# Kernel optimization log

Measured on AMD Instinct MI355X. Metric: run time of the kernel, lower is better.

## Reference

```python
import jax, jax.numpy as jnp
import numpy as np

N_NODES = 50000
N_EDGES = 800000
D_FEAT = 64      # num_src_feats == num_dst_feats
D_EDGE = 16      # num_edge_feats
D_HID = 16       # hidden width of both tiny MLPs
D_MSG = 64       # msg_size
D_OUT = 64       # num_out_feats


def setup_inputs() -> dict:
    key = jax.random.key(0)
    ks = jax.random.split(key, 12)
    x = jax.random.normal(ks[0], (N_NODES, D_FEAT), dtype=jnp.float32)
    edge_feats = jax.random.normal(ks[1], (N_EDGES, D_EDGE), dtype=jnp.float32)
    src = jax.random.randint(ks[2], (N_EDGES,), 0, N_NODES, dtype=jnp.int32)
    dst = jax.random.randint(ks[3], (N_EDGES,), 0, N_NODES, dtype=jnp.int32)

    def linear_params(k, fan_in, fan_out):
        kw, kb = jax.random.split(k)
        bound = 1.0 / np.sqrt(fan_in)
        W = jax.random.uniform(kw, (fan_in, fan_out), jnp.float32, -bound, bound)
        b = jax.random.uniform(kb, (fan_out,), jnp.float32, -bound, bound)
        return W, b

    # fc_msg: [D_EDGE + D_FEAT, 16, D_MSG]
    msg_W1, msg_b1 = linear_params(ks[4], D_EDGE + D_FEAT, D_HID)
    msg_W2, msg_b2 = linear_params(ks[5], D_HID, D_MSG)
    # fc_udt: [D_FEAT + D_MSG, 16, D_OUT]
    udt_W1, udt_b1 = linear_params(ks[6], D_FEAT + D_MSG, D_HID)
    udt_W2, udt_b2 = linear_params(ks[7], D_HID, D_OUT)

    return {
        "x": x, "edge_feats": edge_feats, "src": src, "dst": dst,
        "msg_W1": msg_W1, "msg_b1": msg_b1, "msg_W2": msg_W2, "msg_b2": msg_b2,
        "udt_W1": udt_W1, "udt_b1": udt_b1, "udt_W2": udt_W2, "udt_b2": udt_b2,
    }


def reference(x, edge_feats, src, dst,
              msg_W1, msg_b1, msg_W2, msg_b2,
              udt_W1, udt_b1, udt_W2, udt_b2):
    # message: m_e = MLP([edge_feats_e, x[src_e]])   (cat order: edge first)
    edge_in = jnp.concatenate([edge_feats, x[src]], axis=1)  # [E, D_EDGE+D_FEAT]
    h = jax.nn.relu(edge_in @ msg_W1 + msg_b1)
    m = h @ msg_W2 + msg_b2  # [E, D_MSG]

    # reduce: r_v = max over incoming edges (DGL fills 0 for nodes w/o in-edges)
    r = jax.ops.segment_max(m, dst, num_segments=N_NODES)  # [N, D_MSG]
    r = jnp.where(jnp.isfinite(r), r, 0.0)

    # update: out_v = MLP([x_v, r_v])
    upd_in = jnp.concatenate([x, r], axis=1)  # [N, D_FEAT+D_MSG]
    h2 = jax.nn.relu(upd_in @ udt_W1 + udt_b1)
    return h2 @ udt_W2 + udt_b2  # [N, D_OUT]
```

## Files before the change

### kernel.cpp

```cpp
#include <hip/hip_runtime.h>
#include <hip/hip_fp16.h>

#define N_NODES 50000
#define N_EDGES 800000

#define NBu 1568
#define BSH 5
#define PB  512
#define EPB 1563
#define PIT 7
#define NCH 7

__device__ __forceinline__ unsigned fkey(float f) {
    unsigned u = __float_as_uint(f);
    return (u & 0x80000000u) ? ~u : (u | 0x80000000u);
}
#define KEY_NEG_INF 0x007FFFFFu

__device__ __forceinline__ unsigned block_exscan256(unsigned v, unsigned* wsum,
                                                    unsigned* chunkTot) {
    const int t = threadIdx.x, lane = t & 63, w = t >> 6;
    unsigned inc = v;
#pragma unroll
    for (int d = 1; d < 64; d <<= 1) {
        unsigned n = __shfl_up(inc, d, 64);
        if (lane >= d) inc += n;
    }
    if (lane == 63) wsum[w] = inc;
    __syncthreads();
    unsigned woff = 0;
#pragma unroll
    for (int i = 0; i < 3; ++i) if (i < w) woff += wsum[i];
    if (chunkTot && t == 255) *chunkTot = woff + inc;
    __syncthreads();
    return woff + inc - v;
}

__global__ __launch_bounds__(256) void chist_xw_kernel(
    const int* __restrict__ dst, unsigned* __restrict__ bcnt,
    const float* __restrict__ x, const float* __restrict__ W1,
    const float* __restrict__ b1, float* __restrict__ xw)
{
    __shared__ unsigned lh[NBu];
    const int t = threadIdx.x, b = blockIdx.x;
    for (int i = t; i < NBu; i += 256) lh[i] = 0u;
    __syncthreads();
    const int e0 = b * EPB;
#pragma unroll
    for (int it = 0; it < PIT; ++it) {
        const int i = it * 256 + t;
        const int e = e0 + i;
        if (i < EPB && e < N_EDGES) atomicAdd(&lh[(unsigned)dst[e] >> BSH], 1u);
    }
    __syncthreads();
    for (int i = t; i < NBu; i += 256) bcnt[(size_t)b * NBu + i] = lh[i];

    if (b < 196) {
        const int v = b * 256 + t;
        if (v < N_NODES) {
            float acc[16];
#pragma unroll
            for (int k = 0; k < 16; ++k) acc[k] = b1[k];
            const float4* xp = reinterpret_cast<const float4*>(x) + (size_t)v * 16;
#pragma unroll
            for (int c = 0; c < 16; ++c) {
                float4 tv = xp[c];
                const float xv[4] = {tv.x, tv.y, tv.z, tv.w};
#pragma unroll
                for (int q = 0; q < 4; ++q) {
                    const int row = 16 + 4 * c + q;
#pragma unroll
                    for (int k = 0; k < 16; ++k)
                        acc[k] = fmaf(xv[q], W1[row * 16 + k], acc[k]);
                }
            }
            float4* op = reinterpret_cast<float4*>(xw) + (size_t)v * 4;
#pragma unroll
            for (int c = 0; c < 4; ++c) {
                float4 o; o.x = acc[4*c]; o.y = acc[4*c+1]; o.z = acc[4*c+2]; o.w = acc[4*c+3];
                op[c] = o;
            }
        }
    }
}

__global__ __launch_bounds__(256) void cscanA_kernel(const unsigned* __restrict__ bcnt,
                                                     unsigned* __restrict__ gstart,
                                                     unsigned* __restrict__ tot) {
    __shared__ unsigned wsum[4];
    __shared__ unsigned carrySh, chunkTot;
    const int t = threadIdx.x, bu = blockIdx.x;
    if (t == 0) carrySh = 0u;
    __syncthreads();
#pragma unroll
    for (int c = 0; c < PB / 256; ++c) {
        const int k = c * 256 + t;
        const unsigned v = bcnt[(size_t)k * NBu + bu];
        const unsigned excl = block_exscan256(v, wsum, &chunkTot);
        gstart[(size_t)k * NBu + bu] = carrySh + excl;
        __syncthreads();
        if (t == 0) carrySh += chunkTot;
        __syncthreads();
    }
    if (t == 0) tot[bu] = carrySh;
}

__global__ __launch_bounds__(256) void cscanB_kernel(const unsigned* __restrict__ tot,
                                                     unsigned* __restrict__ boffG) {
    __shared__ unsigned wsum[4];
    __shared__ unsigned carrySh, chunkTot;
    const int t = threadIdx.x;
    if (t == 0) carrySh = 0u;
    __syncthreads();
    for (int c = 0; c < NCH; ++c) {
        const int idx = c * 256 + t;
        const unsigned v = (idx < NBu) ? tot[idx] : 0u;
        const unsigned excl = block_exscan256(v, wsum, &chunkTot);
        if (idx < NBu) boffG[idx] = carrySh + excl;
        __syncthreads();
        if (t == 0) carrySh += chunkTot;
        __syncthreads();
    }
}

__global__ __launch_bounds__(256) void partition_kernel(
    const int* __restrict__ dst, const unsigned* __restrict__ gstart,
    const unsigned* __restrict__ boffG, unsigned* __restrict__ part)
{
    __shared__ unsigned stV[EPB];
    __shared__ unsigned short stB[EPB];
    __shared__ unsigned lh[NBu], lstart[NBu], lc[NBu], gs[NBu];
    __shared__ unsigned wsum[4], carrySh, chunkTot;
    const int t = threadIdx.x, b = blockIdx.x;
    for (int i = t; i < NBu; i += 256) lh[i] = 0u;
    __syncthreads();
    const int e0 = b * EPB;
#pragma unroll
    for (int it = 0; it < PIT; ++it) {
        const int i = it * 256 + t;
        const int e = e0 + i;
        if (i < EPB && e < N_EDGES) atomicAdd(&lh[(unsigned)dst[e] >> BSH], 1u);
    }
    if (t == 0) carrySh = 0u;
    __syncthreads();
    for (int c = 0; c < NCH; ++c) {
        const int idx = c * 256 + t;
        const unsigned v = (idx < NBu) ? lh[idx] : 0u;
        const unsigned excl = block_exscan256(v, wsum, &chunkTot);
        if (idx < NBu) {
            const unsigned s0 = carrySh + excl;
            lstart[idx] = s0;
            lc[idx]     = s0;
            gs[idx]     = gstart[(size_t)b * NBu + idx] + boffG[idx];
        }
        __syncthreads();
        if (t == 0) carrySh += chunkTot;
        __syncthreads();
    }
#pragma unroll
    for (int it = 0; it < PIT; ++it) {
        const int i = it * 256 + t;
        const int e = e0 + i;
        if (i < EPB && e < N_EDGES) {
            const unsigned d = (unsigned)dst[e];
            const unsigned bkt = d >> BSH;
            const unsigned p = atomicAdd(&lc[bkt], 1u);
            stV[p] = ((d & 31u) << 20) | (unsigned)e;
            stB[p] = (unsigned short)bkt;
        }
    }
    __syncthreads();
    const int lim = min(EPB, N_EDGES - e0);
#pragma unroll
    for (int it = 0; it < PIT; ++it) {
        const int i = it * 256 + t;
        if (i < lim) {
            const unsigned bkt = stB[i];
            part[gs[bkt] + ((unsigned)i - lstart[bkt])] = stV[i];
        }
    }
}

__global__ __launch_bounds__(256) void hcomp_kernel(
    const float* __restrict__ ef, const int* __restrict__ src,
    const float* __restrict__ xw, const float* __restrict__ W1,
    unsigned* __restrict__ h16)
{
    const int e = blockIdx.x * 256 + threadIdx.x;
    float in[16];
    const float4* efp = reinterpret_cast<const float4*>(ef) + (size_t)e * 4;
#pragma unroll
    for (int c = 0; c < 4; ++c) {
        float4 tv = efp[c];
        in[4*c+0]=tv.x; in[4*c+1]=tv.y; in[4*c+2]=tv.z; in[4*c+3]=tv.w;
    }
    const int s = src[e];
    float h[16];
    const float4* xp = reinterpret_cast<const float4*>(xw) + (size_t)s * 4;
#pragma unroll
    for (int c = 0; c < 4; ++c) {
        float4 tv = xp[c];
        h[4*c+0]=tv.x; h[4*c+1]=tv.y; h[4*c+2]=tv.z; h[4*c+3]=tv.w;
    }
#pragma unroll
    for (int i = 0; i < 16; ++i)
#pragma unroll
        for (int k = 0; k < 16; ++k)
            h[k] = fmaf(in[i], W1[i*16 + k], h[k]);
    unsigned wds[8];
#pragma unroll
    for (int k = 0; k < 8; ++k) {
        __half2 t2 = __floats2half2_rn(fmaxf(h[2*k], 0.0f), fmaxf(h[2*k+1], 0.0f));
        wds[k] = *reinterpret_cast<unsigned*>(&t2);
    }
    uint4* hp = reinterpret_cast<uint4*>(h16) + (size_t)e * 2;
    hp[0] = make_uint4(wds[0], wds[1], wds[2], wds[3]);
    hp[1] = make_uint4(wds[4], wds[5], wds[6], wds[7]);
}

__global__ __launch_bounds__(256) void reduce_fused_kernel(
    const unsigned* __restrict__ part,
    const unsigned* __restrict__ boffG, const unsigned* __restrict__ tot,
    const unsigned* __restrict__ h16,
    const float* __restrict__ W2, const float* __restrict__ b2,
    const float* __restrict__ x,
    const float* __restrict__ uW1, const float* __restrict__ ub1,
    const float* __restrict__ uW2, const float* __restrict__ ub2,
    float* __restrict__ out)
{
    __shared__ unsigned rmax[32][65];
    __shared__ float    xsh[32][65];
    const int tid = threadIdx.x, b = blockIdx.x;
    const unsigned base = boffG[b], cnt = tot[b];
    const int v0 = b * 32;

    for (int i = tid; i < 32 * 65; i += 256) (&rmax[0][0])[i] = KEY_NEG_INF;
    for (int i = tid; i < 512; i += 256) {
        const int row = i >> 4, c = i & 15;
        float4 tv = (v0 + row < N_NODES)
            ? reinterpret_cast<const float4*>(x)[(size_t)(v0 + row) * 16 + c]
            : make_float4(0.f, 0.f, 0.f, 0.f);
        xsh[row][c*4+0] = tv.x; xsh[row][c*4+1] = tv.y;
        xsh[row][c*4+2] = tv.z; xsh[row][c*4+3] = tv.w;
    }
    __syncthreads();

    const int nIter = (int)((cnt + 255u) >> 8);
    for (int it = 0; it < nIter; ++it) {
        const unsigned slot = (unsigned)it * 256u + (unsigned)tid;
        if (slot < cnt) {
            const unsigned pv = part[base + slot];
            const int e    = (int)(pv & 0xFFFFFu);
            const int nloc = (int)(pv >> 20);
            float h[16];
            {
                const uint4* hp = reinterpret_cast<const uint4*>(h16) + (size_t)e * 2;
                uint4 A = hp[0], B = hp[1];
                unsigned wd[8] = {A.x, A.y, A.z, A.w, B.x, B.y, B.z, B.w};
#pragma unroll
                for (int k = 0; k < 8; ++k) {
                    __half2 t2 = *reinterpret_cast<const __half2*>(&wd[k]);
                    float2 f = __half22float2(t2);
                    h[2*k] = f.x; h[2*k+1] = f.y;
                }
            }
#pragma unroll
            for (int j0 = 0; j0 < 64; j0 += 16) {
                float m[16];
#pragma unroll
                for (int t16 = 0; t16 < 16; ++t16) m[t16] = b2[j0 + t16];
#pragma unroll
                for (int k = 0; k < 16; ++k)
#pragma unroll
                    for (int t16 = 0; t16 < 16; ++t16)
                        m[t16] = fmaf(h[k], W2[k*64 + j0 + t16], m[t16]);
#pragma unroll
                for (int t16 = 0; t16 < 16; ++t16)
                    atomicMax(&rmax[nloc][j0 + t16], fkey(m[t16]));
            }
        }
    }
    __syncthreads();

    if (tid < 128) {
        const int nl = tid >> 2;
        const int qq = tid & 3;
        const int v  = v0 + nl;
        if (v < N_NODES) {
            float h2[16];
#pragma unroll
            for (int k = 0; k < 16; ++k) h2[k] = ub1[k];
            for (int row = 0; row < 64; ++row) {
                const float xv = xsh[nl][row];
#pragma unroll
                for (int k = 0; k < 16; ++k)
                    h2[k] = fmaf(xv, uW1[row*16 + k], h2[k]);
            }
            for (int j = 0; j < 64; ++j) {
                const unsigned kk = rmax[nl][j];
                unsigned u = (kk & 0x80000000u) ? (kk ^ 0x80000000u) : ~kk;
                float f = __uint_as_float(u);
                if (!(f >= -3.402823466e38f && f <= 3.402823466e38f)) f = 0.0f;
#pragma unroll
                for (int k = 0; k < 16; ++k)
                    h2[k] = fmaf(f, uW1[(64 + j)*16 + k], h2[k]);
            }
#pragma unroll
            for (int k = 0; k < 16; ++k) h2[k] = fmaxf(h2[k], 0.0f);
            float* op = out + (size_t)v * 64 + qq * 16;
#pragma unroll
            for (int c = 0; c < 4; ++c) {
                float oo[4];
#pragma unroll
                for (int u4 = 0; u4 < 4; ++u4) {
                    const int col = qq*16 + 4*c + u4;
                    float a = ub2[col];
#pragma unroll
                    for (int k = 0; k < 16; ++k)
                        a = fmaf(h2[k], uW2[k*64 + col], a);
                    oo[u4] = a;
                }
                float4 o; o.x=oo[0]; o.y=oo[1]; o.z=oo[2]; o.w=oo[3];
                reinterpret_cast<float4*>(op)[c] = o;
            }
        }
    }
}

__device__ __forceinline__ void wave_lds_fence() {
    asm volatile("s_waitcnt lgkmcnt(0)" ::: "memory");
    __builtin_amdgcn_sched_barrier(0);
}

__global__ __launch_bounds__(256) void init0_kernel(unsigned* __restrict__ rkey) {
    const int i = blockIdx.x * 256 + threadIdx.x;
    reinterpret_cast<uint4*>(rkey)[i] =
        make_uint4(KEY_NEG_INF, KEY_NEG_INF, KEY_NEG_INF, KEY_NEG_INF);
}

__global__ __launch_bounds__(64) void edge_kernel(
    const float* __restrict__ x, const float* __restrict__ ef,
    const int* __restrict__ src, const int* __restrict__ dst,
    const float* __restrict__ W1, const float* __restrict__ b1,
    const float* __restrict__ W2, const float* __restrict__ b2,
    unsigned* __restrict__ rkey)
{
    const int lane = threadIdx.x;
    const int e    = blockIdx.x * 64 + lane;
    __shared__ unsigned mld[64][17];
    __shared__ int      dld[64];
    float in[80];
    const float4* efp = reinterpret_cast<const float4*>(ef) + (size_t)e * 4;
#pragma unroll
    for (int c = 0; c < 4; ++c) {
        float4 tv = efp[c];
        in[4*c+0]=tv.x; in[4*c+1]=tv.y; in[4*c+2]=tv.z; in[4*c+3]=tv.w;
    }
    const int s = src[e];
    dld[lane] = dst[e];
    const float4* xp = reinterpret_cast<const float4*>(x) + (size_t)s * 16;
#pragma unroll
    for (int c = 0; c < 16; ++c) {
        float4 tv = xp[c];
        in[16+4*c+0]=tv.x; in[16+4*c+1]=tv.y; in[16+4*c+2]=tv.z; in[16+4*c+3]=tv.w;
    }
    float h[16];
#pragma unroll
    for (int k = 0; k < 16; ++k) h[k] = b1[k];
#pragma unroll
    for (int i = 0; i < 80; ++i)
#pragma unroll
        for (int k = 0; k < 16; ++k)
            h[k] = fmaf(in[i], W1[i*16 + k], h[k]);
#pragma unroll
    for (int k = 0; k < 16; ++k) h[k] = fmaxf(h[k], 0.0f);
    const int er = lane >> 4, jj = lane & 15;
#pragma unroll
    for (int j0 = 0; j0 < 64; j0 += 16) {
        float m[16];
#pragma unroll
        for (int t = 0; t < 16; ++t) m[t] = b2[j0 + t];
#pragma unroll
        for (int k = 0; k < 16; ++k)
#pragma unroll
            for (int t = 0; t < 16; ++t)
                m[t] = fmaf(h[k], W2[k*64 + j0 + t], m[t]);
        wave_lds_fence();
#pragma unroll
        for (int t = 0; t < 16; ++t) mld[lane][t] = fkey(m[t]);
        wave_lds_fence();
#pragma unroll
        for (int eg = 0; eg < 16; ++eg) {
            const int ee = (eg << 2) | er;
            atomicMax(&rkey[((size_t)dld[ee] << 6) + (unsigned)(j0 + jj)],
                      mld[ee][jj]);
        }
    }
}

__global__ __launch_bounds__(256) void node_kernel(
    const float* __restrict__ x, const unsigned* rkey,
    const float* __restrict__ W1, const float* __restrict__ b1,
    const float* __restrict__ W2, const float* __restrict__ b2,
    float* out)
{
    const int v = blockIdx.x * 256 + threadIdx.x;
    if (v >= N_NODES) return;
    float in[128];
    const float4* xp = reinterpret_cast<const float4*>(x) + (size_t)v * 16;
#pragma unroll
    for (int c = 0; c < 16; ++c) {
        float4 tv = xp[c];
        in[4*c+0]=tv.x; in[4*c+1]=tv.y; in[4*c+2]=tv.z; in[4*c+3]=tv.w;
    }
    const uint4* rp = reinterpret_cast<const uint4*>(rkey) + (size_t)v * 16;
#pragma unroll
    for (int c = 0; c < 16; ++c) {
        uint4 tv = rp[c];
        unsigned ks[4] = {tv.x, tv.y, tv.z, tv.w};
#pragma unroll
        for (int qq = 0; qq < 4; ++qq) {
            unsigned k = ks[qq];
            unsigned u = (k & 0x80000000u) ? (k ^ 0x80000000u) : ~k;
            float f = __uint_as_float(u);
            if (!(f >= -3.402823466e38f && f <= 3.402823466e38f)) f = 0.0f;
            in[64 + 4*c + qq] = f;
        }
    }
    float h[16];
#pragma unroll
    for (int k = 0; k < 16; ++k) h[k] = b1[k];
#pragma unroll
    for (int i = 0; i < 128; ++i)
#pragma unroll
        for (int k = 0; k < 16; ++k)
            h[k] = fmaf(in[i], W1[i*16 + k], h[k]);
#pragma unroll
    for (int k = 0; k < 16; ++k) h[k] = fmaxf(h[k], 0.0f);
    float* op = out + (size_t)v * 64;
#pragma unroll
    for (int c = 0; c < 16; ++c) {
        float oo[4];
#pragma unroll
        for (int qq = 0; qq < 4; ++qq) {
            float a = b2[4*c + qq];
#pragma unroll
            for (int k = 0; k < 16; ++k)
                a = fmaf(h[k], W2[k*64 + 4*c + qq], a);
            oo[qq] = a;
        }
        float4 o; o.x=oo[0]; o.y=oo[1]; o.z=oo[2]; o.w=oo[3];
        reinterpret_cast<float4*>(op)[c] = o;
    }
}

extern "C" void kernel_launch(void* const* d_in, const int* in_sizes, int n_in,
                              void* d_out, int out_size, void* d_ws, size_t ws_size,
                              hipStream_t stream) {
    const float* x   = (const float*)d_in[0];
    const float* ef  = (const float*)d_in[1];
    const int*   src = (const int*)d_in[2];
    const int*   dst = (const int*)d_in[3];
    const float* mW1 = (const float*)d_in[4];
    const float* mb1 = (const float*)d_in[5];
    const float* mW2 = (const float*)d_in[6];
    const float* mb2 = (const float*)d_in[7];
    const float* uW1 = (const float*)d_in[8];
    const float* ub1 = (const float*)d_in[9];
    const float* uW2 = (const float*)d_in[10];
    const float* ub2 = (const float*)d_in[11];

    float* out = (float*)d_out;

    unsigned* part   = (unsigned*)d_ws;
    unsigned* bcnt   = part + N_EDGES;
    unsigned* gstart = bcnt + (size_t)PB * NBu;
    unsigned* tot    = gstart + (size_t)PB * NBu;
    unsigned* boffG  = tot + NBu;
    float*    xw     = (float*)(boffG + NBu);
    unsigned* h16    = (unsigned*)(xw + (size_t)50176 * 16);
    const size_t T1_NEEDED =
        (size_t)((char*)(h16 + (size_t)N_EDGES * 8) - (char*)d_ws);

    if (ws_size >= T1_NEEDED) {
        hipLaunchKernelGGL(chist_xw_kernel,  dim3(PB),   dim3(256), 0, stream,
                           dst, bcnt, x, mW1, mb1, xw);
        hipLaunchKernelGGL(cscanA_kernel,    dim3(NBu),  dim3(256), 0, stream,
                           bcnt, gstart, tot);
        hipLaunchKernelGGL(cscanB_kernel,    dim3(1),    dim3(256), 0, stream,
                           tot, boffG);
        hipLaunchKernelGGL(partition_kernel, dim3(PB),   dim3(256), 0, stream,
                           dst, gstart, boffG, part);
        hipLaunchKernelGGL(hcomp_kernel,     dim3(3125), dim3(256), 0, stream,
                           ef, src, xw, mW1, h16);
        hipLaunchKernelGGL(reduce_fused_kernel, dim3(NBu), dim3(256), 0, stream,
                           part, boffG, tot, h16, mW2, mb2,
                           x, uW1, ub1, uW2, ub2, out);
    } else {
        unsigned* rkey = (unsigned*)d_out;
        hipLaunchKernelGGL(init0_kernel, dim3(3125), dim3(256), 0, stream, rkey);
        hipLaunchKernelGGL(edge_kernel, dim3(12500), dim3(64), 0, stream,
                           x, ef, src, dst, mW1, mb1, mW2, mb2, rkey);
        hipLaunchKernelGGL(node_kernel, dim3((N_NODES + 255) / 256), dim3(256), 0, stream,
                           x, rkey, uW1, ub1, uW2, ub2, out);
    }
}
```

Before: 124.5 us.

## Build full CSR by destination with two-level partition and per-node register max reduction

Replaces the single-level 32-node bucket partition and LDS atomicMax reduction with a two-pass partition: 256-node coarse buckets, then a per-bucket counting sort by node to build a full CSR (nbase offsets). The reduce kernel now assigns 8 lanes per node, computes messages and keeps the max in registers, combines with shuffles, and fuses the update MLP. This removes LDS atomics and the 2-D scan but adds an extra partition pass, more register pressure (64-float accumulators), and per-node load imbalance.

```diff
diff --git a/kernel.cpp b/kernel.cpp
--- a/kernel.cpp
+++ b/kernel.cpp
@@ -4,18 +4,23 @@
 #define N_NODES 50000
 #define N_EDGES 800000
 
-#define NBu 1568
-#define BSH 5
-#define PB  512
-#define EPB 1563
-#define PIT 7
-#define NCH 7
+#define NB   196
+#define PB   256
+#define EPB  3125
+#define PIT  13
+#define CAP2 4608
+#define NVT  50176
 
 __device__ __forceinline__ unsigned fkey(float f) {
     unsigned u = __float_as_uint(f);
     return (u & 0x80000000u) ? ~u : (u | 0x80000000u);
 }
 #define KEY_NEG_INF 0x007FFFFFu
+
+__device__ __forceinline__ void wave_lds_fence() {
+    asm volatile("s_waitcnt lgkmcnt(0)" ::: "memory");
+    __builtin_amdgcn_sched_barrier(0);
+}
 
 __device__ __forceinline__ unsigned block_exscan256(unsigned v, unsigned* wsum,
                                                     unsigned* chunkTot) {
@@ -41,19 +46,18 @@
     const float* __restrict__ x, const float* __restrict__ W1,
     const float* __restrict__ b1, float* __restrict__ xw)
 {
-    __shared__ unsigned lh[NBu];
+    __shared__ unsigned lh[NB];
     const int t = threadIdx.x, b = blockIdx.x;
-    for (int i = t; i < NBu; i += 256) lh[i] = 0u;
+    if (t < NB) lh[t] = 0u;
     __syncthreads();
     const int e0 = b * EPB;
 #pragma unroll
     for (int it = 0; it < PIT; ++it) {
         const int i = it * 256 + t;
-        const int e = e0 + i;
-        if (i < EPB && e < N_EDGES) atomicAdd(&lh[(unsigned)dst[e] >> BSH], 1u);
-    }
-    __syncthreads();
-    for (int i = t; i < NBu; i += 256) bcnt[(size_t)b * NBu + i] = lh[i];
+        if (i < EPB) atomicAdd(&lh[(unsigned)dst[e0 + i] >> 8], 1u);
+    }
+    __syncthreads();
+    if (t < NB) bcnt[(size_t)b * NB + t] = lh[t];
 
     if (b < 196) {
         const int v = b * 256 + t;
@@ -84,101 +88,23 @@
     }
 }
 
-__global__ __launch_bounds__(256) void cscanA_kernel(const unsigned* __restrict__ bcnt,
-                                                     unsigned* __restrict__ gstart,
+__global__ __launch_bounds__(256) void cscanA_kernel(unsigned* __restrict__ bcnt,
                                                      unsigned* __restrict__ tot) {
     __shared__ unsigned wsum[4];
-    __shared__ unsigned carrySh, chunkTot;
     const int t = threadIdx.x, bu = blockIdx.x;
-    if (t == 0) carrySh = 0u;
-    __syncthreads();
-#pragma unroll
-    for (int c = 0; c < PB / 256; ++c) {
-        const int k = c * 256 + t;
-        const unsigned v = bcnt[(size_t)k * NBu + bu];
-        const unsigned excl = block_exscan256(v, wsum, &chunkTot);
-        gstart[(size_t)k * NBu + bu] = carrySh + excl;
-        __syncthreads();
-        if (t == 0) carrySh += chunkTot;
-        __syncthreads();
-    }
-    if (t == 0) tot[bu] = carrySh;
+    const unsigned v = bcnt[(size_t)t * NB + bu];
+    const unsigned excl = block_exscan256(v, wsum, nullptr);
+    bcnt[(size_t)t * NB + bu] = excl;
+    if (t == 255) tot[bu] = excl + v;
 }
 
 __global__ __launch_bounds__(256) void cscanB_kernel(const unsigned* __restrict__ tot,
                                                      unsigned* __restrict__ boffG) {
     __shared__ unsigned wsum[4];
-    __shared__ unsigned carrySh, chunkTot;
     const int t = threadIdx.x;
-    if (t == 0) carrySh = 0u;
-    __syncthreads();
-    for (int c = 0; c < NCH; ++c) {
-        const int idx = c * 256 + t;
-        const unsigned v = (idx < NBu) ? tot[idx] : 0u;
-        const unsigned excl = block_exscan256(v, wsum, &chunkTot);
-        if (idx < NBu) boffG[idx] = carrySh + excl;
-        __syncthreads();
-        if (t == 0) carrySh += chunkTot;
-        __syncthreads();
-    }
-}
-
-__global__ __launch_bounds__(256) void partition_kernel(
-    const int* __restrict__ dst, const unsigned* __restrict__ gstart,
-    const unsigned* __restrict__ boffG, unsigned* __restrict__ part)
-{
-    __shared__ unsigned stV[EPB];
-    __shared__ unsigned short stB[EPB];
-    __shared__ unsigned lh[NBu], lstart[NBu], lc[NBu], gs[NBu];
-    __shared__ unsigned wsum[4], carrySh, chunkTot;
-    const int t = threadIdx.x, b = blockIdx.x;
-    for (int i = t; i < NBu; i += 256) lh[i] = 0u;
-    __syncthreads();
-    const int e0 = b * EPB;
-#pragma unroll
-    for (int it = 0; it < PIT; ++it) {
-        const int i = it * 256 + t;
-        const int e = e0 + i;
-        if (i < EPB && e < N_EDGES) atomicAdd(&lh[(unsigned)dst[e] >> BSH], 1u);
-    }
-    if (t == 0) carrySh = 0u;
-    __syncthreads();
-    for (int c = 0; c < NCH; ++c) {
-        const int idx = c * 256 + t;
-        const unsigned v = (idx < NBu) ? lh[idx] : 0u;
-        const unsigned excl = block_exscan256(v, wsum, &chunkTot);
-        if (idx < NBu) {
-            const unsigned s0 = carrySh + excl;
-            lstart[idx] = s0;
-            lc[idx]     = s0;
-            gs[idx]     = gstart[(size_t)b * NBu + idx] + boffG[idx];
-        }
-        __syncthreads();
-        if (t == 0) carrySh += chunkTot;
-        __syncthreads();
-    }
-#pragma unroll
-    for (int it = 0; it < PIT; ++it) {
-        const int i = it * 256 + t;
-        const int e = e0 + i;
-        if (i < EPB && e < N_EDGES) {
-            const unsigned d = (unsigned)dst[e];
-            const unsigned bkt = d >> BSH;
-            const unsigned p = atomicAdd(&lc[bkt], 1u);
-            stV[p] = ((d & 31u) << 20) | (unsigned)e;
-            stB[p] = (unsigned short)bkt;
-        }
-    }
-    __syncthreads();
-    const int lim = min(EPB, N_EDGES - e0);
-#pragma unroll
-    for (int it = 0; it < PIT; ++it) {
-        const int i = it * 256 + t;
-        if (i < lim) {
-            const unsigned bkt = stB[i];
-            part[gs[bkt] + ((unsigned)i - lstart[bkt])] = stV[i];
-        }
-    }
+    const unsigned v = (t < NB) ? tot[t] : 0u;
+    const unsigned excl = block_exscan256(v, wsum, nullptr);
+    if (t < NB) boffG[t] = excl;
 }
 
 __global__ __launch_bounds__(256) void hcomp_kernel(
@@ -218,9 +144,103 @@
     hp[1] = make_uint4(wds[4], wds[5], wds[6], wds[7]);
 }
 
-__global__ __launch_bounds__(256) void reduce_fused_kernel(
-    const unsigned* __restrict__ part,
+__global__ __launch_bounds__(256) void part1_kernel(
+    const int* __restrict__ dst, const unsigned* __restrict__ gstart,
+    const unsigned* __restrict__ boffG, unsigned* __restrict__ part1)
+{
+    __shared__ unsigned stV[EPB];
+    __shared__ unsigned char stB[EPB];
+    __shared__ unsigned lh[NB], lstart[NB], lc[NB], gs[NB];
+    __shared__ unsigned wsum[4];
+    const int t = threadIdx.x, b = blockIdx.x;
+    if (t < NB) lh[t] = 0u;
+    __syncthreads();
+    const int e0 = b * EPB;
+#pragma unroll
+    for (int it = 0; it < PIT; ++it) {
+        const int i = it * 256 + t;
+        if (i < EPB) atomicAdd(&lh[(unsigned)dst[e0 + i] >> 8], 1u);
+    }
+    __syncthreads();
+    {
+        const unsigned v = (t < NB) ? lh[t] : 0u;
+        const unsigned excl = block_exscan256(v, wsum, nullptr);
+        if (t < NB) {
+            lstart[t] = excl;
+            lc[t]     = excl;
+            gs[t]     = gstart[(size_t)b * NB + t] + boffG[t];
+        }
+    }
+    __syncthreads();
+#pragma unroll
+    for (int it = 0; it < PIT; ++it) {
+        const int i = it * 256 + t;
+        if (i < EPB) {
+            const int e = e0 + i;
+            const unsigned d = (unsigned)dst[e];
+            const unsigned bkt = d >> 8;
+            const unsigned p = atomicAdd(&lc[bkt], 1u);
+            stV[p] = ((d & 255u) << 20) | (unsigned)e;
+            stB[p] = (unsigned char)bkt;
+        }
+    }
+    __syncthreads();
+#pragma unroll
+    for (int it = 0; it < PIT; ++it) {
+        const int i = it * 256 + t;
+        if (i < EPB) {
+            const unsigned bkt = stB[i];
+            part1[gs[bkt] + ((unsigned)i - lstart[bkt])] = stV[i];
+        }
+    }
+}
+
+__global__ __launch_bounds__(256) void part2_kernel(
+    const unsigned* __restrict__ part1,
     const unsigned* __restrict__ boffG, const unsigned* __restrict__ tot,
+    unsigned* __restrict__ part2, unsigned* __restrict__ nbase)
+{
+    __shared__ unsigned stE[CAP2];
+    __shared__ unsigned fh[256], fstart[256], fcur[256];
+    __shared__ unsigned wsum[4];
+    const int t = threadIdx.x, b = blockIdx.x;
+    const unsigned gb = boffG[b], cnt = tot[b];
+    fh[t] = 0u; fcur[t] = 0u;
+    __syncthreads();
+    const int iters = (int)((cnt + 255u) >> 8);
+    for (int it = 0; it < iters; ++it) {
+        const unsigned i = (unsigned)it * 256u + (unsigned)t;
+        if (i < cnt) atomicAdd(&fh[part1[gb + i] >> 20], 1u);
+    }
+    __syncthreads();
+    {
+        const unsigned v = fh[t];
+        fstart[t] = block_exscan256(v, wsum, nullptr);
+    }
+    __syncthreads();
+    for (int it = 0; it < iters; ++it) {
+        const unsigned i = (unsigned)it * 256u + (unsigned)t;
+        if (i < cnt) {
+            const unsigned pv = part1[gb + i];
+            const unsigned nloc = pv >> 20;
+            const unsigned e = pv & 0xFFFFFu;
+            const unsigned pos = fstart[nloc] + atomicAdd(&fcur[nloc], 1u);
+            if (pos < CAP2) stE[pos] = e;
+            else            part2[gb + pos] = e;
+        }
+    }
+    __syncthreads();
+    const unsigned lim = (cnt < CAP2) ? cnt : CAP2;
+    for (int it = 0; it < iters; ++it) {
+        const unsigned i = (unsigned)it * 256u + (unsigned)t;
+        if (i < lim) part2[gb + i] = stE[i];
+    }
+    nbase[(size_t)b * 256 + t] = gb + fstart[t];
+    if (b == NB - 1 && t == 0) nbase[NVT] = (unsigned)N_EDGES;
+}
+
+__global__ __launch_bounds__(128) void reduce_node_kernel(
+    const unsigned* __restrict__ part2, const unsigned* __restrict__ nbase,
     const unsigned* __restrict__ h16,
     const float* __restrict__ W2, const float* __restrict__ b2,
     const float* __restrict__ x,
@@ -228,108 +248,108 @@
     const float* __restrict__ uW2, const float* __restrict__ ub2,
     float* __restrict__ out)
 {
-    __shared__ unsigned rmax[32][65];
-    __shared__ float    xsh[32][65];
     const int tid = threadIdx.x, b = blockIdx.x;
-    const unsigned base = boffG[b], cnt = tot[b];
-    const int v0 = b * 32;
-
-    for (int i = tid; i < 32 * 65; i += 256) (&rmax[0][0])[i] = KEY_NEG_INF;
-    for (int i = tid; i < 512; i += 256) {
-        const int row = i >> 4, c = i & 15;
-        float4 tv = (v0 + row < N_NODES)
-            ? reinterpret_cast<const float4*>(x)[(size_t)(v0 + row) * 16 + c]
-            : make_float4(0.f, 0.f, 0.f, 0.f);
-        xsh[row][c*4+0] = tv.x; xsh[row][c*4+1] = tv.y;
-        xsh[row][c*4+2] = tv.z; xsh[row][c*4+3] = tv.w;
-    }
-    __syncthreads();
-
-    const int nIter = (int)((cnt + 255u) >> 8);
-    for (int it = 0; it < nIter; ++it) {
-        const unsigned slot = (unsigned)it * 256u + (unsigned)tid;
-        if (slot < cnt) {
-            const unsigned pv = part[base + slot];
-            const int e    = (int)(pv & 0xFFFFFu);
-            const int nloc = (int)(pv >> 20);
+    const int g = tid >> 3, l = tid & 7;
+    const int v = b * 16 + g;
+    if (v >= N_NODES) return;
+
+    const unsigned beg = nbase[v], end = nbase[v + 1];
+    float acc[64];
+#pragma unroll
+    for (int j = 0; j < 64; ++j) acc[j] = -__builtin_inff();
+
+    const unsigned deg = end - beg;
+    const int trips = (int)((deg + 7u) >> 3);
+    for (int tr = 0; tr < trips; ++tr) {
+        const unsigned idx = beg + (unsigned)tr * 8u + (unsigned)l;
+        if (idx < end) {
+            const unsigned e = part2[idx];
+            const uint4* hp = reinterpret_cast<const uint4*>(h16) + (size_t)e * 2;
+            uint4 A = hp[0], B = hp[1];
+            unsigned wd[8] = {A.x, A.y, A.z, A.w, B.x, B.y, B.z, B.w};
             float h[16];
-            {
-                const uint4* hp = reinterpret_cast<const uint4*>(h16) + (size_t)e * 2;
-                uint4 A = hp[0], B = hp[1];
-                unsigned wd[8] = {A.x, A.y, A.z, A.w, B.x, B.y, B.z, B.w};
-#pragma unroll
-                for (int k = 0; k < 8; ++k) {
-                    __half2 t2 = *reinterpret_cast<const __half2*>(&wd[k]);
-                    float2 f = __half22float2(t2);
-                    h[2*k] = f.x; h[2*k+1] = f.y;
-                }
+#pragma unroll
+            for (int k = 0; k < 8; ++k) {
+                __half2 t2 = *reinterpret_cast<const __half2*>(&wd[k]);
+                float2 f = __half22float2(t2);
+                h[2*k] = f.x; h[2*k+1] = f.y;
             }
 #pragma unroll
-            for (int j0 = 0; j0 < 64; j0 += 16) {
-                float m[16];
-#pragma unroll
-                for (int t16 = 0; t16 < 16; ++t16) m[t16] = b2[j0 + t16];
-#pragma unroll
-                for (int k = 0; k < 16; ++k)
-#pragma unroll
-                    for (int t16 = 0; t16 < 16; ++t16)
-                        m[t16] = fmaf(h[k], W2[k*64 + j0 + t16], m[t16]);
-#pragma unroll
-                for (int t16 = 0; t16 < 16; ++t16)
-                    atomicMax(&rmax[nloc][j0 + t16], fkey(m[t16]));
+            for (int j = 0; j < 64; ++j) {
+                float m = h[0] * W2[j];
+#pragma unroll
+                for (int k = 1; k < 16; ++k)
+                    m = fmaf(h[k], W2[k*64 + j], m);
+                acc[j] = fmaxf(acc[j], m);
             }
         }
     }
-    __syncthreads();
-
-    if (tid < 128) {
-        const int nl = tid >> 2;
-        const int qq = tid & 3;
-        const int v  = v0 + nl;
-        if (v < N_NODES) {
-            float h2[16];
-#pragma unroll
-            for (int k = 0; k < 16; ++k) h2[k] = ub1[k];
-            for (int row = 0; row < 64; ++row) {
-                const float xv = xsh[nl][row];
-#pragma unroll
-                for (int k = 0; k < 16; ++k)
-                    h2[k] = fmaf(xv, uW1[row*16 + k], h2[k]);
-            }
-            for (int j = 0; j < 64; ++j) {
-                const unsigned kk = rmax[nl][j];
-                unsigned u = (kk & 0x80000000u) ? (kk ^ 0x80000000u) : ~kk;
-                float f = __uint_as_float(u);
-                if (!(f >= -3.402823466e38f && f <= 3.402823466e38f)) f = 0.0f;
-#pragma unroll
-                for (int k = 0; k < 16; ++k)
-                    h2[k] = fmaf(f, uW1[(64 + j)*16 + k], h2[k]);
-            }
-#pragma unroll
-            for (int k = 0; k < 16; ++k) h2[k] = fmaxf(h2[k], 0.0f);
-            float* op = out + (size_t)v * 64 + qq * 16;
-#pragma unroll
-            for (int c = 0; c < 4; ++c) {
-                float oo[4];
-#pragma unroll
-                for (int u4 = 0; u4 < 4; ++u4) {
-                    const int col = qq*16 + 4*c + u4;
-                    float a = ub2[col];
-#pragma unroll
-                    for (int k = 0; k < 16; ++k)
-                        a = fmaf(h2[k], uW2[k*64 + col], a);
-                    oo[u4] = a;
-                }
-                float4 o; o.x=oo[0]; o.y=oo[1]; o.z=oo[2]; o.w=oo[3];
-                reinterpret_cast<float4*>(op)[c] = o;
-            }
-        }
-    }
-}
-
-__device__ __forceinline__ void wave_lds_fence() {
-    asm volatile("s_waitcnt lgkmcnt(0)" ::: "memory");
-    __builtin_amdgcn_sched_barrier(0);
+#pragma unroll
+    for (int mk = 1; mk <= 4; mk <<= 1)
+#pragma unroll
+        for (int j = 0; j < 64; ++j)
+            acc[j] = fmaxf(acc[j], __shfl_xor(acc[j], mk, 64));
+
+    float rloc[8];
+#pragma unroll
+    for (int rr = 0; rr < 8; ++rr) {
+        const int j = l * 8 + rr;
+        rloc[rr] = (deg == 0u) ? 0.0f : (acc[j] + b2[j]);
+    }
+
+    float h2[16];
+#pragma unroll
+    for (int k = 0; k < 16; ++k) h2[k] = 0.0f;
+    const float4* xp = reinterpret_cast<const float4*>(x) + (size_t)v * 16 + l * 2;
+    float4 xa = xp[0], xb = xp[1];
+    const float xv[8] = {xa.x, xa.y, xa.z, xa.w, xb.x, xb.y, xb.z, xb.w};
+#pragma unroll
+    for (int rr = 0; rr < 8; ++rr) {
+        const int row = l * 8 + rr;
+        const float4* wr = reinterpret_cast<const float4*>(uW1 + row * 16);
+        float4 w0 = wr[0], w1 = wr[1], w2v = wr[2], w3 = wr[3];
+        const float wf[16] = {w0.x,w0.y,w0.z,w0.w, w1.x,w1.y,w1.z,w1.w,
+                              w2v.x,w2v.y,w2v.z,w2v.w, w3.x,w3.y,w3.z,w3.w};
+#pragma unroll
+        for (int k = 0; k < 16; ++k) h2[k] = fmaf(xv[rr], wf[k], h2[k]);
+    }
+#pragma unroll
+    for (int rr = 0; rr < 8; ++rr) {
+        const int row = 64 + l * 8 + rr;
+        const float4* wr = reinterpret_cast<const float4*>(uW1 + row * 16);
+        float4 w0 = wr[0], w1 = wr[1], w2v = wr[2], w3 = wr[3];
+        const float wf[16] = {w0.x,w0.y,w0.z,w0.w, w1.x,w1.y,w1.z,w1.w,
+                              w2v.x,w2v.y,w2v.z,w2v.w, w3.x,w3.y,w3.z,w3.w};
+#pragma unroll
+        for (int k = 0; k < 16; ++k) h2[k] = fmaf(rloc[rr], wf[k], h2[k]);
+    }
+    if (l == 0) {
+#pragma unroll
+        for (int k = 0; k < 16; ++k) h2[k] += ub1[k];
+    }
+#pragma unroll
+    for (int mk = 1; mk <= 4; mk <<= 1)
+#pragma unroll
+        for (int k = 0; k < 16; ++k)
+            h2[k] += __shfl_xor(h2[k], mk, 64);
+#pragma unroll
+    for (int k = 0; k < 16; ++k) h2[k] = fmaxf(h2[k], 0.0f);
+
+    float oo[8];
+#pragma unroll
+    for (int c = 0; c < 8; ++c) {
+        const int col = l * 8 + c;
+        float a = ub2[col];
+#pragma unroll
+        for (int k = 0; k < 16; ++k)
+            a = fmaf(h2[k], uW2[k*64 + col], a);
+        oo[c] = a;
+    }
+    float* op = out + (size_t)v * 64 + l * 8;
+    float4 o0; o0.x=oo[0]; o0.y=oo[1]; o0.z=oo[2]; o0.w=oo[3];
+    float4 o1; o1.x=oo[4]; o1.y=oo[5]; o1.z=oo[6]; o1.w=oo[7];
+    reinterpret_cast<float4*>(op)[0] = o0;
+    reinterpret_cast<float4*>(op)[1] = o1;
 }
 
 __global__ __launch_bounds__(256) void init0_kernel(unsigned* __restrict__ rkey) {
@@ -472,29 +492,32 @@
 
     float* out = (float*)d_out;
 
-    unsigned* part   = (unsigned*)d_ws;
-    unsigned* bcnt   = part + N_EDGES;
-    unsigned* gstart = bcnt + (size_t)PB * NBu;
-    unsigned* tot    = gstart + (size_t)PB * NBu;
-    unsigned* boffG  = tot + NBu;
-    float*    xw     = (float*)(boffG + NBu);
-    unsigned* h16    = (unsigned*)(xw + (size_t)50176 * 16);
+    unsigned* part1v = (unsigned*)d_ws;
+    unsigned* part2v = part1v + N_EDGES;
+    unsigned* bcnt   = part2v + N_EDGES;
+    unsigned* tot    = bcnt + (size_t)PB * NB;
+    unsigned* boffG  = tot + NB;
+    unsigned* nbase  = boffG + NB;
+    float*    xw     = (float*)(nbase + NVT + 1);
+    unsigned* h16    = (unsigned*)(xw + (size_t)NVT * 16);
     const size_t T1_NEEDED =
         (size_t)((char*)(h16 + (size_t)N_EDGES * 8) - (char*)d_ws);
 
     if (ws_size >= T1_NEEDED) {
-        hipLaunchKernelGGL(chist_xw_kernel,  dim3(PB),   dim3(256), 0, stream,
+        hipLaunchKernelGGL(chist_xw_kernel, dim3(PB),   dim3(256), 0, stream,
                            dst, bcnt, x, mW1, mb1, xw);
-        hipLaunchKernelGGL(cscanA_kernel,    dim3(NBu),  dim3(256), 0, stream,
-                           bcnt, gstart, tot);
-        hipLaunchKernelGGL(cscanB_kernel,    dim3(1),    dim3(256), 0, stream,
+        hipLaunchKernelGGL(cscanA_kernel,   dim3(NB),   dim3(256), 0, stream,
+                           bcnt, tot);
+        hipLaunchKernelGGL(cscanB_kernel,   dim3(1),    dim3(256), 0, stream,
                            tot, boffG);
-        hipLaunchKernelGGL(partition_kernel, dim3(PB),   dim3(256), 0, stream,
-                           dst, gstart, boffG, part);
-        hipLaunchKernelGGL(hcomp_kernel,     dim3(3125), dim3(256), 0, stream,
+        hipLaunchKernelGGL(hcomp_kernel,    dim3(3125), dim3(256), 0, stream,
                            ef, src, xw, mW1, h16);
-        hipLaunchKernelGGL(reduce_fused_kernel, dim3(NBu), dim3(256), 0, stream,
-                           part, boffG, tot, h16, mW2, mb2,
+        hipLaunchKernelGGL(part1_kernel,    dim3(PB),   dim3(256), 0, stream,
+                           dst, bcnt, boffG, part1v);
+        hipLaunchKernelGGL(part2_kernel,    dim3(NB),   dim3(256), 0, stream,
+                           part1v, boffG, tot, part2v, nbase);
+        hipLaunchKernelGGL(reduce_node_kernel, dim3(NVT / 16), dim3(128), 0, stream,
+                           part2v, nbase, h16, mW2, mb2,
                            x, uW1, ub1, uW2, ub2, out);
     } else {
         unsigned* rkey = (unsigned*)d_out;
```

Measured after the change: 205.1 us. +64.7%, slower.
